# Optimization experiments

Hardware: AMD Instinct MI355X
Metric: run time of the kernel (lower is better)

The kernel has to match this reference:

```python
import jax, jax.numpy as jnp
import numpy as np

# Llama-3-8B-style attention config (from init_kwargs)
DIM = 4096
N_HEADS = 32
N_KV_HEADS = 8
HEAD_DIM = DIM // N_HEADS          # 128
N_REP = N_HEADS // N_KV_HEADS      # 4 (GQA replication)
ROPE_THETA = 10000.0
W_SCALE = 0.02


def setup_inputs() -> dict:
    key = jax.random.key(0)
    kx, kq, kk, kv, ko = jax.random.split(key, 5)
    bsz, seqlen = 1, 2048
    x = jax.random.normal(kx, (bsz, seqlen, DIM), dtype=jnp.float32)
    # nn.Linear(in, out, bias=False) -> store as [in, out] so y = x @ W
    wq = jax.random.normal(kq, (DIM, N_HEADS * HEAD_DIM), dtype=jnp.float32) * W_SCALE
    wk = jax.random.normal(kk, (DIM, N_KV_HEADS * HEAD_DIM), dtype=jnp.float32) * W_SCALE
    wv = jax.random.normal(kv, (DIM, N_KV_HEADS * HEAD_DIM), dtype=jnp.float32) * W_SCALE
    wo = jax.random.normal(ko, (N_HEADS * HEAD_DIM, DIM), dtype=jnp.float32) * W_SCALE
    return {"x": x, "wq": wq, "wk": wk, "wv": wv, "wo": wo, "start_pos": 0}


def _rope_cos_sin(seqlen: int):
    # precompute_freqs_cis: freqs[j] = theta^(-2j/dim), angles = outer(t, freqs)
    inv_freq = 1.0 / (ROPE_THETA ** (jnp.arange(0, HEAD_DIM, 2, dtype=jnp.float32) / HEAD_DIM))
    angles = jnp.arange(seqlen, dtype=jnp.float32)[:, None] * inv_freq[None, :]  # [s, hd/2]
    return jnp.cos(angles), jnp.sin(angles)


def _apply_rope(t, cos, sin):
    # t: [b, s, h, hd]; pairs (even, odd) form complex numbers, rotate by angle
    tr, ti = t[..., 0::2], t[..., 1::2]
    c = cos[None, :, None, :]
    s = sin[None, :, None, :]
    out = jnp.stack([tr * c - ti * s, tr * s + ti * c], axis=-1)  # [b,s,h,hd/2,2]
    return out.reshape(t.shape)


def reference(x, wq, wk, wv, wo, start_pos):
    bsz, seqlen, _ = x.shape
    xq = (x @ wq).reshape(bsz, seqlen, N_HEADS, HEAD_DIM)
    xk = (x @ wk).reshape(bsz, seqlen, N_KV_HEADS, HEAD_DIM)
    xv = (x @ wv).reshape(bsz, seqlen, N_KV_HEADS, HEAD_DIM)

    cos, sin = _rope_cos_sin(seqlen)
    xq = _apply_rope(xq, cos, sin)
    xk = _apply_rope(xk, cos, sin)

    # GQA: repeat_interleave KV heads to match query heads
    xk = jnp.repeat(xk, N_REP, axis=2)
    xv = jnp.repeat(xv, N_REP, axis=2)

    scale = 1.0 / jnp.sqrt(jnp.float32(HEAD_DIM))
    scores = jnp.einsum('bqhd,bkhd->bhqk', xq, xk) * scale  # [b,h,s,s]
    causal = jnp.tril(jnp.ones((seqlen, seqlen), dtype=bool))
    scores = jnp.where(causal[None, None], scores, -jnp.inf)
    probs = jax.nn.softmax(scores, axis=-1)

    out = jnp.einsum('bhqk,bkhd->bqhd', probs, xv)
    out = out.reshape(bsz, seqlen, N_HEADS * HEAD_DIM)
    return out @ wo
```

## Files before the change

### kernel.cpp

```cpp
#include <hip/hip_runtime.h>
#include <stdint.h>

typedef __attribute__((ext_vector_type(8))) short bf16x8;
typedef __attribute__((ext_vector_type(4))) short bf16x4;
typedef __attribute__((ext_vector_type(4))) float f32x4;
typedef __attribute__((ext_vector_type(4))) unsigned short u16x4;

#define DIM   4096
#define SEQ   2048
#define NH    32
#define NKV   8
#define HD    128
#define QKV_N 6144
#define ATT_SCALE 0.08838834764831845f

static __device__ __forceinline__ unsigned short f2bf_bits(float f) {
  uint32_t x = __builtin_bit_cast(uint32_t, f);
  x += 0x7fffu + ((x >> 16) & 1u);
  return (unsigned short)(x >> 16);
}
static __device__ __forceinline__ float bf_bits2f(unsigned short u) {
  uint32_t x = ((uint32_t)u) << 16;
  return __builtin_bit_cast(float, x);
}

static __device__ __forceinline__ void g2l16(const unsigned short* gp,
                                             unsigned short* lp) {
  __builtin_amdgcn_global_load_lds(
      (const __attribute__((address_space(1))) unsigned int*)gp,
      (__attribute__((address_space(3))) unsigned int*)lp, 16, 0, 0);
}

__global__ __launch_bounds__(256) void transpose_f32_bf16(
    const float* __restrict__ in, unsigned short* __restrict__ out,
    int ld_in, int ld_out) {
  __shared__ unsigned short sh[32][33];
  const int c0 = blockIdx.x * 32, r0 = blockIdx.y * 32;
  const int t = threadIdx.x;
  const int cc = t & 31, rr = (t >> 5) * 4;
#pragma unroll
  for (int p = 0; p < 4; ++p)
    sh[cc][rr + p] = f2bf_bits(in[(size_t)(r0 + rr + p) * ld_in + (c0 + cc)]);
  __syncthreads();
#pragma unroll
  for (int p = 0; p < 4; ++p)
    out[(size_t)(c0 + rr + p) * ld_out + (r0 + cc)] = sh[rr + p][cc];
}

__global__ __launch_bounds__(256) void transpose_bf16(
    const unsigned short* __restrict__ in, unsigned short* __restrict__ out,
    int ld_in, int ld_out) {
  __shared__ unsigned short sh[32][33];
  const int c0 = blockIdx.x * 32, r0 = blockIdx.y * 32;
  const int t = threadIdx.x;
  const int cc = t & 31, rr = (t >> 5) * 4;
#pragma unroll
  for (int p = 0; p < 4; ++p)
    sh[cc][rr + p] = in[(size_t)(r0 + rr + p) * ld_in + (c0 + cc)];
  __syncthreads();
#pragma unroll
  for (int p = 0; p < 4; ++p)
    out[(size_t)(c0 + rr + p) * ld_out + (r0 + cc)] = sh[rr + p][cc];
}

__global__ __launch_bounds__(256) void convert_f32_bf16(
    const float* __restrict__ in, unsigned short* __restrict__ out) {
  const int i = (blockIdx.x * 256 + threadIdx.x) * 4;
  const float4 v = *(const float4*)&in[i];
  u16x4 w;
  w[0] = f2bf_bits(v.x); w[1] = f2bf_bits(v.y);
  w[2] = f2bf_bits(v.z); w[3] = f2bf_bits(v.w);
  *(u16x4*)&out[i] = w;
}

#define BM 128
#define BN 128
#define BK 64

template <bool OUT_FP32>
__global__ __launch_bounds__(256) void gemm_bt(
    const unsigned short* __restrict__ A, int lda,
    const unsigned short* __restrict__ Bt, int ldb,
    void* __restrict__ C_, int ldc, int K) {
  __shared__ __align__(16) unsigned short ldsA[BM * BK];
  __shared__ __align__(16) unsigned short ldsB[BN * BK];
  const int t = threadIdx.x;
  const int wave = t >> 6, lane = t & 63;
  const int lane16 = lane & 15, quad = lane >> 4;
  const int m0 = blockIdx.y * BM, n0 = blockIdx.x * BN;
  const int wrow = (wave >> 1) * 64, wcol = (wave & 1) * 64;

  f32x4 acc[4][4];
#pragma unroll
  for (int i = 0; i < 4; ++i)
#pragma unroll
    for (int j = 0; j < 4; ++j) acc[i][j] = (f32x4){0.f, 0.f, 0.f, 0.f};

  const int srow = t >> 3;
  const int scol = ((t & 7) * 8) ^ ((srow & 7) << 3);
  size_t arow[4], brow[4];
#pragma unroll
  for (int p = 0; p < 4; ++p) {
    arow[p] = (size_t)(m0 + p * 32 + srow) * lda + scol;
    brow[p] = (size_t)(n0 + p * 32 + srow) * ldb + scol;
  }
  const int rsw = (lane16 & 7) << 3;

  for (int kk = 0; kk < K; kk += BK) {
    __syncthreads();
#pragma unroll
    for (int p = 0; p < 4; ++p) {
      g2l16(&A[arow[p] + kk],  &ldsA[p * 2048 + t * 8]);
      g2l16(&Bt[brow[p] + kk], &ldsB[p * 2048 + t * 8]);
    }
    __syncthreads();

#pragma unroll
    for (int c = 0; c < 2; ++c) {
      bf16x8 af[4], bfr[4];
#pragma unroll
      for (int mi = 0; mi < 4; ++mi)
        af[mi] = *(const bf16x8*)
            &ldsA[(wrow + mi * 16 + lane16) * BK + ((c * 32 + quad * 8) ^ rsw)];
#pragma unroll
      for (int ni = 0; ni < 4; ++ni)
        bfr[ni] = *(const bf16x8*)
            &ldsB[(wcol + ni * 16 + lane16) * BK + ((c * 32 + quad * 8) ^ rsw)];
#pragma unroll
      for (int mi = 0; mi < 4; ++mi)
#pragma unroll
        for (int ni = 0; ni < 4; ++ni)
          acc[mi][ni] = __builtin_amdgcn_mfma_f32_16x16x32_bf16(
              af[mi], bfr[ni], acc[mi][ni], 0, 0, 0);
    }
  }

#pragma unroll
  for (int mi = 0; mi < 4; ++mi)
#pragma unroll
    for (int ni = 0; ni < 4; ++ni)
#pragma unroll
      for (int r = 0; r < 4; ++r) {
        const int row = m0 + wrow + mi * 16 + quad * 4 + r;
        const int col = n0 + wcol + ni * 16 + lane16;
        if (OUT_FP32)
          ((float*)C_)[(size_t)row * ldc + col] = acc[mi][ni][r];
        else
          ((unsigned short*)C_)[(size_t)row * ldc + col] = f2bf_bits(acc[mi][ni][r]);
      }
}

__global__ __launch_bounds__(256) void rope_kernel(unsigned short* __restrict__ qkv) {
  const int idx = blockIdx.x * 256 + threadIdx.x;
  const int pos = idx / 2560;
  const int rem = idx - pos * 2560;
  const int head = rem >> 6;
  const int i = rem & 63;
  const float inv_freq = __expf(-(float)(2 * i) * (9.210340371976184f / 128.0f));
  const float ang = (float)pos * inv_freq;
  float s, c;
  __sincosf(ang, &s, &c);
  const int col = (head < 32) ? head * 128 + 2 * i
                              : 4096 + (head - 32) * 128 + 2 * i;
  unsigned short* p = qkv + (size_t)pos * QKV_N + col;
  const float tr = bf_bits2f(p[0]), ti = bf_bits2f(p[1]);
  p[0] = f2bf_bits(tr * c - ti * s);
  p[1] = f2bf_bits(tr * s + ti * c);
}

#define QT 64
#define KT 64
#define KLS (HD + 8)
#define NQ  (SEQ / QT)
#define DEFER_THR 8.0f

__global__ __launch_bounds__(256) void attn_kernel(
    const unsigned short* __restrict__ qkv,
    const unsigned short* __restrict__ vT,
    unsigned short* __restrict__ attn) {
  __shared__ __align__(16) unsigned short kls[KT][KLS];
  __shared__ __align__(16) unsigned short vls[HD][KT];

  const int t = threadIdx.x;
  const int wave = t >> 6, lane = t & 63;
  const int lane16 = lane & 15, quad = lane >> 4;
  const int h = blockIdx.y, kvh = h >> 2;
  const unsigned short* kbase = qkv + 4096 + kvh * HD;
  const unsigned short* vbase = vT + (size_t)kvh * HD * SEQ;

  const int kr = t >> 2, kc = (t & 3) * 8;
  const int vd = t >> 1;
  const int vu0 = (t & 1) * 8;
  const int vswz = (vd & 7) << 1;
  const int rswz = (lane16 & 7) << 1;
  const unsigned short* ksrc0 = &kbase[(size_t)kr * QKV_N + kc];
  const unsigned short* vsrc0 = &vbase[(size_t)vd * SEQ + (t & 1) * 32];

  bf16x8 kreg[4], vreg[4];

  for (int half = 0; half < 2; ++half) {
    const int qt = half ? (int)blockIdx.x : (NQ - 1 - (int)blockIdx.x);
    const int q0 = qt * QT;
    const int wq0 = q0 + wave * 16;
    const int qrow = wq0 + lane16;
    const int nkb = qt + 1;

#pragma unroll
    for (int j = 0; j < 4; ++j) kreg[j] = *(const bf16x8*)&ksrc0[j * 32];
#pragma unroll
    for (int j = 0; j < 4; ++j) vreg[j] = *(const bf16x8*)&vsrc0[j * 8];

    const unsigned short* qbase = qkv + (size_t)wq0 * QKV_N + h * HD;

    bf16x8 qf[4];
#pragma unroll
    for (int dc = 0; dc < 4; ++dc)
      qf[dc] = *(const bf16x8*)&qbase[(size_t)lane16 * QKV_N + dc * 32 + quad * 8];

    f32x4 o[8];
#pragma unroll
    for (int i = 0; i < 8; ++i) o[i] = (f32x4){0.f, 0.f, 0.f, 0.f};
    float m = -INFINITY, l = 0.f;

    for (int kb = 0; kb < nkb; ++kb) {
      const int key0 = kb * KT;
      __syncthreads();

#pragma unroll
      for (int j = 0; j < 4; ++j)
        *(bf16x8*)&kls[kr][kc + j * 32] = kreg[j];
#pragma unroll
      for (int j = 0; j < 4; ++j)
        *(bf16x8*)&vls[vd][((vu0 + j * 2) ^ vswz) * 4] = vreg[j];

      if (kb + 1 < nkb) {
        const unsigned short* ks = ksrc0 + (size_t)(kb + 1) * KT * QKV_N;
        const unsigned short* vs = vsrc0 + (kb + 1) * KT;
#pragma unroll
        for (int j = 0; j < 4; ++j) kreg[j] = *(const bf16x8*)&ks[j * 32];
#pragma unroll
        for (int j = 0; j < 4; ++j) vreg[j] = *(const bf16x8*)&vs[j * 8];
      }

      asm volatile("s_waitcnt lgkmcnt(0)" ::: "memory");
      __builtin_amdgcn_s_barrier();

      f32x4 S[4];
      __builtin_amdgcn_s_setprio(1);
#pragma unroll
      for (int kt = 0; kt < 4; ++kt) {
        f32x4 sacc = (f32x4){0.f, 0.f, 0.f, 0.f};
#pragma unroll
        for (int dc = 0; dc < 4; ++dc) {
          const bf16x8 kf = *(const bf16x8*)&kls[kt * 16 + lane16][dc * 32 + quad * 8];
          sacc = __builtin_amdgcn_mfma_f32_16x16x32_bf16(kf, qf[dc], sacc, 0, 0, 0);
        }
        S[kt] = sacc;
      }
      __builtin_amdgcn_s_setprio(0);

      float sv[4][4], mx = -INFINITY;
#pragma unroll
      for (int kt = 0; kt < 4; ++kt)
#pragma unroll
        for (int r = 0; r < 4; ++r) {
          const int key = key0 + kt * 16 + quad * 4 + r;
          sv[kt][r] = (key <= qrow) ? S[kt][r] * ATT_SCALE : -INFINITY;
          mx = fmaxf(mx, sv[kt][r]);
        }
      mx = fmaxf(mx, __shfl_xor(mx, 16, 64));
      mx = fmaxf(mx, __shfl_xor(mx, 32, 64));

      const bool skip = __all(mx <= m + DEFER_THR);
      float alpha = 1.f;
      if (!skip) {
        const float newm = fmaxf(m, mx);
        alpha = __expf(m - newm);
        m = newm;
      }
      float p[4][4], rs = 0.f;
#pragma unroll
      for (int kt = 0; kt < 4; ++kt)
#pragma unroll
        for (int r = 0; r < 4; ++r) {
          p[kt][r] = __expf(sv[kt][r] - m);
          rs += p[kt][r];
        }
      rs += __shfl_xor(rs, 16, 64);
      rs += __shfl_xor(rs, 32, 64);
      if (skip) {
        l += rs;
      } else {
        l = l * alpha + rs;
#pragma unroll
        for (int dt = 0; dt < 8; ++dt)
#pragma unroll
          for (int r = 0; r < 4; ++r) o[dt][r] *= alpha;
      }

      bf16x4 pb[4];
#pragma unroll
      for (int kt = 0; kt < 4; ++kt) {
        bf16x4 w;
        w[0] = (short)f2bf_bits(p[kt][0]); w[1] = (short)f2bf_bits(p[kt][1]);
        w[2] = (short)f2bf_bits(p[kt][2]); w[3] = (short)f2bf_bits(p[kt][3]);
        pb[kt] = w;
      }

      __builtin_amdgcn_s_setprio(1);
#pragma unroll
      for (int dt = 0; dt < 8; ++dt)
#pragma unroll
        for (int kt = 0; kt < 4; ++kt) {
          const bf16x4 vf = *(const bf16x4*)
              &vls[dt * 16 + lane16][(((kt * 4 + quad) ^ rswz)) * 4];
          o[dt] = __builtin_amdgcn_mfma_f32_16x16x16bf16_1k(vf, pb[kt], o[dt], 0, 0, 0);
        }
      __builtin_amdgcn_s_setprio(0);
    }

    const float inv_l = 1.0f / l;
    unsigned short* dst = attn + (size_t)qrow * DIM + h * HD;
#pragma unroll
    for (int dt = 0; dt < 8; ++dt) {
      u16x4 w;
#pragma unroll
      for (int r = 0; r < 4; ++r) w[r] = f2bf_bits(o[dt][r] * inv_l);
      *(u16x4*)&dst[dt * 16 + quad * 4] = w;
    }
  }
}

extern "C" void kernel_launch(void* const* d_in, const int* in_sizes, int n_in,
                              void* d_out, int out_size, void* d_ws, size_t ws_size,
                              hipStream_t stream) {
  const float* x  = (const float*)d_in[0];
  const float* wq = (const float*)d_in[1];
  const float* wk = (const float*)d_in[2];
  const float* wv = (const float*)d_in[3];
  const float* wo = (const float*)d_in[4];
  float* out = (float*)d_out;

  unsigned short* wqkvT = (unsigned short*)d_ws;
  unsigned short* woT   = wqkvT;
  unsigned short* qkv   = wqkvT + (size_t)6144 * 4096;
  unsigned short* vT    = qkv   + (size_t)2048 * 6144;
  unsigned short* attn  = vT    + (size_t)1024 * 2048;
  unsigned short* xb    = attn;

  const dim3 b256(256);
  transpose_f32_bf16<<<dim3(128, 128), b256, 0, stream>>>(wq, wqkvT, 4096, 4096);
  transpose_f32_bf16<<<dim3(32, 128),  b256, 0, stream>>>(wk, wqkvT + (size_t)4096 * 4096, 1024, 4096);
  transpose_f32_bf16<<<dim3(32, 128),  b256, 0, stream>>>(wv, wqkvT + (size_t)5120 * 4096, 1024, 4096);
  convert_f32_bf16<<<dim3(SEQ * DIM / 1024), b256, 0, stream>>>(x, xb);

  gemm_bt<false><<<dim3(QKV_N / BN, SEQ / BM), b256, 0, stream>>>(
      xb, DIM, wqkvT, DIM, qkv, QKV_N, DIM);

  rope_kernel<<<dim3((SEQ * 2560) / 256), b256, 0, stream>>>(qkv);

  transpose_bf16<<<dim3(32, 64), b256, 0, stream>>>(qkv + 5120, vT, 6144, 2048);

  attn_kernel<<<dim3(NQ / 2, NH), b256, 0, stream>>>(qkv, vT, attn);

  transpose_f32_bf16<<<dim3(128, 128), b256, 0, stream>>>(wo, woT, 4096, 4096);

  gemm_bt<true><<<dim3(DIM / BN, SEQ / BM), b256, 0, stream>>>(
      attn, DIM, woT, DIM, out, DIM, DIM);
}
```

Measured before the change: 502.5 us.

## Vectorize weight transpose, fold attention scale into RoPE, skip mask on full tiles

```diff
diff --git a/kernel.cpp b/kernel.cpp
--- a/kernel.cpp
+++ b/kernel.cpp
@@ -34,17 +34,29 @@
 __global__ __launch_bounds__(256) void transpose_f32_bf16(
     const float* __restrict__ in, unsigned short* __restrict__ out,
     int ld_in, int ld_out) {
-  __shared__ unsigned short sh[32][33];
-  const int c0 = blockIdx.x * 32, r0 = blockIdx.y * 32;
+  __shared__ unsigned short sh[64][66];
+  const int c0 = blockIdx.x * 64, r0 = blockIdx.y * 64;
   const int t = threadIdx.x;
-  const int cc = t & 31, rr = (t >> 5) * 4;
-#pragma unroll
-  for (int p = 0; p < 4; ++p)
-    sh[cc][rr + p] = f2bf_bits(in[(size_t)(r0 + rr + p) * ld_in + (c0 + cc)]);
+  const int tc = (t & 15) * 4;
+  const int tr = t >> 4;
+#pragma unroll
+  for (int i = 0; i < 4; ++i) {
+    const int r = tr + i * 16;
+    const float4 v = *(const float4*)&in[(size_t)(r0 + r) * ld_in + c0 + tc];
+    u16x4 w;
+    w[0] = f2bf_bits(v.x); w[1] = f2bf_bits(v.y);
+    w[2] = f2bf_bits(v.z); w[3] = f2bf_bits(v.w);
+    *(u16x4*)&sh[r][tc] = w;
+  }
   __syncthreads();
 #pragma unroll
-  for (int p = 0; p < 4; ++p)
-    out[(size_t)(c0 + rr + p) * ld_out + (r0 + cc)] = sh[rr + p][cc];
+  for (int i = 0; i < 4; ++i) {
+    const int c = tr + i * 16;
+    u16x4 w;
+#pragma unroll
+    for (int j = 0; j < 4; ++j) w[j] = sh[tc + j][c];
+    *(u16x4*)&out[(size_t)(c0 + c) * ld_out + r0 + tc] = w;
+  }
 }
 
 __global__ __launch_bounds__(256) void transpose_bf16(
@@ -160,12 +172,14 @@
   const float ang = (float)pos * inv_freq;
   float s, c;
   __sincosf(ang, &s, &c);
-  const int col = (head < 32) ? head * 128 + 2 * i
-                              : 4096 + (head - 32) * 128 + 2 * i;
+  const bool isq = (head < 32);
+  const float g = isq ? ATT_SCALE : 1.0f;
+  const int col = isq ? head * 128 + 2 * i
+                      : 4096 + (head - 32) * 128 + 2 * i;
   unsigned short* p = qkv + (size_t)pos * QKV_N + col;
   const float tr = bf_bits2f(p[0]), ti = bf_bits2f(p[1]);
-  p[0] = f2bf_bits(tr * c - ti * s);
-  p[1] = f2bf_bits(tr * s + ti * c);
+  p[0] = f2bf_bits((tr * c - ti * s) * g);
+  p[1] = f2bf_bits((tr * s + ti * c) * g);
 }
 
 #define QT 64
@@ -260,14 +274,24 @@
       __builtin_amdgcn_s_setprio(0);
 
       float sv[4][4], mx = -INFINITY;
-#pragma unroll
-      for (int kt = 0; kt < 4; ++kt)
-#pragma unroll
-        for (int r = 0; r < 4; ++r) {
-          const int key = key0 + kt * 16 + quad * 4 + r;
-          sv[kt][r] = (key <= qrow) ? S[kt][r] * ATT_SCALE : -INFINITY;
-          mx = fmaxf(mx, sv[kt][r]);
-        }
+      if (key0 + (KT - 1) <= wq0) {
+#pragma unroll
+        for (int kt = 0; kt < 4; ++kt)
+#pragma unroll
+          for (int r = 0; r < 4; ++r) {
+            sv[kt][r] = S[kt][r];
+            mx = fmaxf(mx, sv[kt][r]);
+          }
+      } else {
+#pragma unroll
+        for (int kt = 0; kt < 4; ++kt)
+#pragma unroll
+          for (int r = 0; r < 4; ++r) {
+            const int key = key0 + kt * 16 + quad * 4 + r;
+            sv[kt][r] = (key <= qrow) ? S[kt][r] : -INFINITY;
+            mx = fmaxf(mx, sv[kt][r]);
+          }
+      }
       mx = fmaxf(mx, __shfl_xor(mx, 16, 64));
       mx = fmaxf(mx, __shfl_xor(mx, 32, 64));
 
@@ -349,9 +373,9 @@
   unsigned short* xb    = attn;
 
   const dim3 b256(256);
-  transpose_f32_bf16<<<dim3(128, 128), b256, 0, stream>>>(wq, wqkvT, 4096, 4096);
-  transpose_f32_bf16<<<dim3(32, 128),  b256, 0, stream>>>(wk, wqkvT + (size_t)4096 * 4096, 1024, 4096);
-  transpose_f32_bf16<<<dim3(32, 128),  b256, 0, stream>>>(wv, wqkvT + (size_t)5120 * 4096, 1024, 4096);
+  transpose_f32_bf16<<<dim3(64, 64), b256, 0, stream>>>(wq, wqkvT, 4096, 4096);
+  transpose_f32_bf16<<<dim3(16, 64), b256, 0, stream>>>(wk, wqkvT + (size_t)4096 * 4096, 1024, 4096);
+  transpose_f32_bf16<<<dim3(16, 64), b256, 0, stream>>>(wv, wqkvT + (size_t)5120 * 4096, 1024, 4096);
   convert_f32_bf16<<<dim3(SEQ * DIM / 1024), b256, 0, stream>>>(x, xb);
 
   gemm_bt<false><<<dim3(QKV_N / BN, SEQ / BM), b256, 0, stream>>>(
@@ -363,7 +387,7 @@
 
   attn_kernel<<<dim3(NQ / 2, NH), b256, 0, stream>>>(qkv, vT, attn);
 
-  transpose_f32_bf16<<<dim3(128, 128), b256, 0, stream>>>(wo, woT, 4096, 4096);
+  transpose_f32_bf16<<<dim3(64, 64), b256, 0, stream>>>(wo, woT, 4096, 4096);
 
   gemm_bt<true><<<dim3(DIM / BN, SEQ / BM), b256, 0, stream>>>(
       attn, DIM, woT, DIM, out, DIM, DIM);
```

Result: no change. 508.3 us (+1.1%).
